# Performance work log

Measured on AMD Instinct MI355X. Metric: run time of the kernel, lower is better.

## Reference

```python
import jax, jax.numpy as jnp
import numpy as np

EPS = 1e-6      # l2_norm / denom clamp eps
BN_EPS = 1e-5   # BatchNorm eps


def _l2norm(x):
    # torch.norm(p=2, dim=-2, keepdim=True).clamp_min(eps)
    n = jnp.sqrt(jnp.sum(x * x, axis=-2, keepdims=True))
    return x / jnp.maximum(n, EPS)


def setup_inputs() -> dict:
    key = jax.random.key(0)
    ks = jax.random.split(key, 9)
    B, Cin_each, Co, H, W = 4, 256, 256, 128, 128
    Cq = Co // 8  # in_places // scale
    Cin = 4 * Cin_each
    return {
        "s5": jax.random.normal(ks[0], (B, Cin_each, H, W), jnp.float32),
        "s4": jax.random.normal(ks[1], (B, Cin_each, H, W), jnp.float32),
        "s3": jax.random.normal(ks[2], (B, Cin_each, H, W), jnp.float32),
        "s2": jax.random.normal(ks[3], (B, Cin_each, H, W), jnp.float32),
        # ConvBnRelu: 1x1 conv (no bias) + BN affine params
        "w_conv": jax.random.normal(ks[4], (Co, Cin), jnp.float32) * 0.03,
        "bn_gamma": jnp.ones((Co,), jnp.float32),
        "bn_beta": jnp.zeros((Co,), jnp.float32),
        # Attention 1x1 convs (with bias)
        "wq": jax.random.normal(ks[5], (Cq, Co), jnp.float32) * 0.06,
        "bq": jnp.zeros((Cq,), jnp.float32),
        "wk": jax.random.normal(ks[6], (Cq, Co), jnp.float32) * 0.06,
        "bk": jnp.zeros((Cq,), jnp.float32),
        "wv": jax.random.normal(ks[7], (Co, Co), jnp.float32) * 0.06,
        "bv": jnp.zeros((Co,), jnp.float32),
        # gamma is Parameter(zeros(1)) in the source; set nonzero so the
        # attention branch contributes to the output for kernel testing.
        "gamma": jnp.array(0.5, jnp.float32),
    }


def reference(s5, s4, s3, s2, w_conv, bn_gamma, bn_beta,
              wq, bq, wk, bk, wv, bv, gamma):
    # --- ConvBnRelu (1x1 conv, train-mode BN, ReLU) ---
    fcat = jnp.concatenate([s5, s4, s3, s2], axis=1)            # [B, 4C, H, W]
    x = jnp.einsum('oc,bchw->bohw', w_conv, fcat)               # 1x1 conv
    mu = x.mean(axis=(0, 2, 3), keepdims=True)
    var = x.var(axis=(0, 2, 3), keepdims=True)                  # biased, as torch BN
    x = (x - mu) / jnp.sqrt(var + BN_EPS)
    x = x * bn_gamma[None, :, None, None] + bn_beta[None, :, None, None]
    feat = jax.nn.relu(x)                                       # [B, C, H, W]

    # --- linear Attention (L2-norm QK, KV trick, no softmax) ---
    B, C, H, W = feat.shape
    N = H * W
    X = feat.reshape(B, C, N)
    Q = jnp.einsum('qc,bcn->bqn', wq, X) + bq[None, :, None]    # [B, Cq, N]
    K = jnp.einsum('qc,bcn->bqn', wk, X) + bk[None, :, None]    # [B, Cq, N]
    V = jnp.einsum('oc,bcn->bon', wv, X) + bv[None, :, None]    # [B, C, N]

    Qn = _l2norm(Q)                                             # norm over channel dim
    Kn = _l2norm(K)

    # denom: N + Q . sum_n K
    e = jnp.einsum('bqn,bq->bn', Qn, Kn.sum(axis=-1))           # [B, N]
    tailor = 1.0 / jnp.maximum(jnp.asarray(N, Qn.dtype) + e, 1e-6)

    # KV trick: [B, Cq, C] then project back through Q
    matrix = jnp.einsum('bqn,bcn->bqc', Kn, V)                  # [B, Cq, C]
    matrix_sum = V.sum(axis=-1)[:, :, None] + \
        jnp.einsum('bqn,bqc->bcn', Qn, matrix)                  # [B, C, N]

    weight_value = matrix_sum * tailor[:, None, :]              # [B, C, N]
    out = gamma * weight_value.reshape(B, C, H, W)
    out = jnp.nan_to_num(out, nan=0.0, posinf=1.0, neginf=-1.0)

    return out + feat
```

## Files before the change

kernel.cpp:

```cpp
#include <hip/hip_runtime.h>

#define B_   4
#define CO   256
#define CIN  1024
#define CQ   32
#define HN   16384
#define NPIX 65536
#define NTOT ((size_t)B_ * CO * HN)

typedef unsigned short ushort_t;
typedef __attribute__((ext_vector_type(8))) short bf16x8;
typedef __attribute__((ext_vector_type(4))) float f32x4;

__device__ __forceinline__ unsigned bf16pair(float x, float y) {
    unsigned xu = __float_as_uint(x), yu = __float_as_uint(y);
    unsigned xr = (xu + 0x7FFFu + ((xu >> 16) & 1u)) >> 16;
    unsigned yr = (yu + 0x7FFFu + ((yu >> 16) & 1u)) >> 16;
    return xr | (yr << 16);
}
__device__ __forceinline__ ushort_t bf16of(float x) {
    unsigned u = __float_as_uint(x);
    return (ushort_t)((u + 0x7FFFu + ((u >> 16) & 1u)) >> 16);
}
__device__ __forceinline__ float bf2f(ushort_t h) {
    return __uint_as_float(((unsigned)h) << 16);
}
__device__ __forceinline__ void unpack8(uint4 u, float* f) {
    f[0] = __uint_as_float(u.x << 16); f[1] = __uint_as_float(u.x & 0xffff0000u);
    f[2] = __uint_as_float(u.y << 16); f[3] = __uint_as_float(u.y & 0xffff0000u);
    f[4] = __uint_as_float(u.z << 16); f[5] = __uint_as_float(u.z & 0xffff0000u);
    f[6] = __uint_as_float(u.w << 16); f[7] = __uint_as_float(u.w & 0xffff0000u);
}
__device__ __forceinline__ void async16(void* lds, const void* g) {
    __builtin_amdgcn_global_load_lds(
        (const __attribute__((address_space(1))) void*)g,
        (__attribute__((address_space(3))) void*)lds, 16, 0, 0);
}

__global__ __launch_bounds__(256) void wcvt(
    const float* __restrict__ w, const float* __restrict__ wq,
    const float* __restrict__ wk, const float* __restrict__ wv,
    ushort_t* __restrict__ w_bf, ushort_t* __restrict__ wqk_bf,
    ushort_t* __restrict__ wv_bf)
{
    int i = blockIdx.x * 256 + threadIdx.x;
    if (i < 262144) {
        w_bf[i] = bf16of(w[i]);
    } else if (i < 278528) {
        int l = i - 262144; int row = l >> 8, col = l & 255;
        float v = (row < 32) ? wq[row * 256 + col] : wk[(row - 32) * 256 + col];
        wqk_bf[l] = bf16of(v);
    } else {
        int l = i - 278528;
        wv_bf[l] = bf16of(wv[l]);
    }
}

__global__ __launch_bounds__(256) void conv_mfma2(
    const float* __restrict__ s5, const float* __restrict__ s4,
    const float* __restrict__ s3, const float* __restrict__ s2,
    const ushort_t* __restrict__ w_bf, ushort_t* __restrict__ xb)
{
    __shared__ ushort_t Aw[128 * 32];
    __shared__ ushort_t Bf[32 * 130];
    const int o0 = blockIdx.x * 128;
    const int n0 = blockIdx.y * 128;
    const int b  = blockIdx.z;
    const int tid = threadIdx.x;
    const int wave = tid >> 6, lane = tid & 63, l15 = lane & 15, quad = lane >> 4;
    const int wm = wave & 1, wn = wave >> 1;
    f32x4 acc[4][4] = {};

    for (int k0 = 0; k0 < CIN; k0 += 32) {
        #pragma unroll
        for (int r = 0; r < 2; ++r) {
            int row = r * 64 + wave * 16;
            const ushort_t* g = w_bf + (size_t)(o0 + row + (lane >> 2)) * CIN
                                + k0 + (lane & 3) * 8;
            async16(&Aw[row * 32], g);
        }
        const int t = k0 >> 8;
        const float* src = ((t == 0) ? s5 : (t == 1) ? s4 : (t == 2) ? s3 : s2)
                           + ((size_t)b * 256 + (k0 & 255)) * HN + n0;
        #pragma unroll
        for (int i = 0; i < 4; ++i) {
            int gi = tid + 256 * i;
            int k = gi >> 5, n4 = gi & 31;
            float4 u = *(const float4*)(src + (size_t)k * HN + n4 * 4);
            *(unsigned*)&Bf[k * 130 + n4 * 4]     = bf16pair(u.x, u.y);
            *(unsigned*)&Bf[k * 130 + n4 * 4 + 2] = bf16pair(u.z, u.w);
        }
        __syncthreads();
        bf16x8 af[4], bfv[4];
        #pragma unroll
        for (int tm = 0; tm < 4; ++tm)
            af[tm] = *(const bf16x8*)&Aw[(wm * 64 + tm * 16 + l15) * 32 + quad * 8];
        #pragma unroll
        for (int tn = 0; tn < 4; ++tn) {
            int nl = wn * 64 + tn * 16 + l15;
            bf16x8 bb;
            #pragma unroll
            for (int j = 0; j < 8; ++j) bb[j] = (short)Bf[(quad * 8 + j) * 130 + nl];
            bfv[tn] = bb;
        }
        #pragma unroll
        for (int tm = 0; tm < 4; ++tm)
            #pragma unroll
            for (int tn = 0; tn < 4; ++tn)
                acc[tm][tn] = __builtin_amdgcn_mfma_f32_16x16x32_bf16(
                    af[tm], bfv[tn], acc[tm][tn], 0, 0, 0);
        __syncthreads();
    }
    #pragma unroll
    for (int tm = 0; tm < 4; ++tm)
        #pragma unroll
        for (int r = 0; r < 4; ++r) {
            int o = o0 + wm * 64 + tm * 16 + quad * 4 + r;
            size_t base = ((size_t)b * CO + o) * HN + n0;
            #pragma unroll
            for (int tn = 0; tn < 4; ++tn)
                xb[base + wn * 64 + tn * 16 + l15] = bf16of(acc[tm][tn][r]);
        }
}

__global__ __launch_bounds__(256) void bn_stats(
    const ushort_t* __restrict__ xb, float* __restrict__ accum)
{
    const int o = blockIdx.x, seg = blockIdx.y, tid = threadIdx.x;
    const int wave = tid >> 6, lane = tid & 63;
    float s = 0.f, ss = 0.f;
    for (int b = 0; b < B_; ++b) {
        const ushort_t* p = xb + ((size_t)(b * CO + o)) * HN + seg * 2048 + tid * 8;
        uint4 u = *(const uint4*)p;
        float f[8]; unpack8(u, f);
        #pragma unroll
        for (int j = 0; j < 8; ++j) { s += f[j]; ss += f[j] * f[j]; }
    }
    #pragma unroll
    for (int m = 1; m < 64; m <<= 1) { s += __shfl_xor(s, m); ss += __shfl_xor(ss, m); }
    __shared__ float shs[4], shss[4];
    if (lane == 0) { shs[wave] = s; shss[wave] = ss; }
    __syncthreads();
    if (tid == 0) {
        atomicAdd(&accum[o],       shs[0] + shs[1] + shs[2] + shs[3]);
        atomicAdd(&accum[256 + o], shss[0] + shss[1] + shss[2] + shss[3]);
    }
}

__global__ __launch_bounds__(256) void bn_finalize(
    const float* __restrict__ accum, const float* __restrict__ g,
    const float* __restrict__ bt, float* __restrict__ scale,
    float* __restrict__ shift)
{
    int o = threadIdx.x;
    float mu  = accum[o] / (float)NPIX;
    float var = accum[256 + o] / (float)NPIX - mu * mu;
    float sc  = g[o] * rsqrtf(var + 1e-5f);
    scale[o] = sc;
    shift[o] = bt[o] - mu * sc;
}

__global__ __launch_bounds__(256) void bnrelu_t(
    const ushort_t* __restrict__ xb, const float* __restrict__ scale,
    const float* __restrict__ shift, ushort_t* __restrict__ featT)
{
    __shared__ ushort_t sh[64 * 68];
    const int hn0 = blockIdx.x * 64, c0 = blockIdx.y * 64, b = blockIdx.z;
    const int tid = threadIdx.x;
    {
        int cl = tid >> 2, seg = tid & 3;
        float sc = scale[c0 + cl], sf = shift[c0 + cl];
        const ushort_t* src = xb + ((size_t)(b * CO + c0 + cl)) * HN + hn0 + seg * 16;
        #pragma unroll
        for (int h = 0; h < 2; ++h) {
            uint4 u = *(const uint4*)(src + h * 8);
            float f[8]; unpack8(u, f);
            #pragma unroll
            for (int j = 0; j < 8; ++j) {
                float v = fmaxf(fmaf(sc, f[j], sf), 0.f);
                sh[(seg * 16 + h * 8 + j) * 68 + cl] = bf16of(v);
            }
        }
    }
    __syncthreads();
    {
        int nl = tid >> 2, seg = tid & 3;
        size_t gn = (size_t)b * HN + hn0 + nl;
        ushort_t* dst = featT + gn * CO + c0 + seg * 16;
        #pragma unroll
        for (int j = 0; j < 4; ++j)
            *(uint2*)(dst + j * 4) = *(const uint2*)&sh[nl * 68 + seg * 16 + j * 4];
    }
}

__global__ __launch_bounds__(256) void qk_mfma(
    const ushort_t* __restrict__ featT, const ushort_t* __restrict__ wqk_bf,
    const float* __restrict__ bq, const float* __restrict__ bk,
    ushort_t* __restrict__ Qt, ushort_t* __restrict__ Kt,
    float* __restrict__ Ksum)
{
    __shared__ ushort_t At[128 * 32];
    __shared__ ushort_t Bt[64 * 32];
    const int n0 = blockIdx.x * 128;
    const int b  = n0 >> 14;
    const int tid = threadIdx.x;
    const int wave = tid >> 6, lane = tid & 63, l15 = lane & 15, quad = lane >> 4;
    const int nsub = (wave & 1) * 64;
    const int isK  = wave >> 1;
    f32x4 acc[4][2] = {};

    for (int k0 = 0; k0 < CO; k0 += 32) {
        #pragma unroll
        for (int r = 0; r < 2; ++r) {
            int row = r * 64 + wave * 16;
            const ushort_t* g = featT + (size_t)(n0 + row + (lane >> 2)) * CO
                                + k0 + (lane & 3) * 8;
            async16(&At[row * 32], g);
        }
        {
            int row = wave * 16;
            const ushort_t* g = wqk_bf + (size_t)(row + (lane >> 2)) * CO
                                + k0 + (lane & 3) * 8;
            async16(&Bt[row * 32], g);
        }
        __syncthreads();
        bf16x8 af[4], bfv[2];
        #pragma unroll
        for (int tm = 0; tm < 4; ++tm)
            af[tm] = *(const bf16x8*)&At[(nsub + tm * 16 + l15) * 32 + quad * 8];
        #pragma unroll
        for (int tc = 0; tc < 2; ++tc)
            bfv[tc] = *(const bf16x8*)&Bt[(isK * 32 + tc * 16 + l15) * 32 + quad * 8];
        #pragma unroll
        for (int tm = 0; tm < 4; ++tm)
            #pragma unroll
            for (int tc = 0; tc < 2; ++tc)
                acc[tm][tc] = __builtin_amdgcn_mfma_f32_16x16x32_bf16(
                    af[tm], bfv[tc], acc[tm][tc], 0, 0, 0);
        __syncthreads();
    }
    const float bias0 = isK ? bk[l15]      : bq[l15];
    const float bias1 = isK ? bk[16 + l15] : bq[16 + l15];
    ushort_t* dst = isK ? Kt : Qt;
    float ks0 = 0.f, ks1 = 0.f;
    #pragma unroll
    for (int tm = 0; tm < 4; ++tm)
        #pragma unroll
        for (int r = 0; r < 4; ++r) {
            float v0 = acc[tm][0][r] + bias0;
            float v1 = acc[tm][1][r] + bias1;
            float sq = v0 * v0 + v1 * v1;
            sq += __shfl_xor(sq, 1); sq += __shfl_xor(sq, 2);
            sq += __shfl_xor(sq, 4); sq += __shfl_xor(sq, 8);
            float inv = 1.f / fmaxf(sqrtf(sq), 1e-6f);
            v0 *= inv; v1 *= inv;
            int n = n0 + nsub + tm * 16 + quad * 4 + r;
            dst[(size_t)n * CQ + l15]      = bf16of(v0);
            dst[(size_t)n * CQ + 16 + l15] = bf16of(v1);
            ks0 += v0; ks1 += v1;
        }
    if (isK) {
        ks0 += __shfl_xor(ks0, 16); ks0 += __shfl_xor(ks0, 32);
        ks1 += __shfl_xor(ks1, 16); ks1 += __shfl_xor(ks1, 32);
        if (quad == 0) {
            atomicAdd(&Ksum[b * CQ + l15],      ks0);
            atomicAdd(&Ksum[b * CQ + 16 + l15], ks1);
        }
    }
}

__global__ __launch_bounds__(256) void v_mfma2(
    const ushort_t* __restrict__ featT, const ushort_t* __restrict__ wv_bf,
    const float* __restrict__ bv, ushort_t* __restrict__ Vt,
    float* __restrict__ Vsum)
{
    __shared__ ushort_t At[128 * 32];
    __shared__ ushort_t Bt[128 * 32];
    const int n0  = blockIdx.x * 128;
    const int co0 = blockIdx.y * 128;
    const int b   = n0 >> 14;
    const int tid = threadIdx.x;
    const int wave = tid >> 6, lane = tid & 63, l15 = lane & 15, quad = lane >> 4;
    const int wm = wave & 1, wn = wave >> 1;
    f32x4 acc[4][4] = {};

    for (int k0 = 0; k0 < CO; k0 += 32) {
        #pragma unroll
        for (int r = 0; r < 2; ++r) {
            int row = r * 64 + wave * 16;
            const ushort_t* ga = featT + (size_t)(n0 + row + (lane >> 2)) * CO
                                 + k0 + (lane & 3) * 8;
            async16(&At[row * 32], ga);
            const ushort_t* gb = wv_bf + (size_t)(co0 + row + (lane >> 2)) * CO
                                 + k0 + (lane & 3) * 8;
            async16(&Bt[row * 32], gb);
        }
        __syncthreads();
        bf16x8 af[4], bfv[4];
        #pragma unroll
        for (int tm = 0; tm < 4; ++tm)
            af[tm] = *(const bf16x8*)&At[(wm * 64 + tm * 16 + l15) * 32 + quad * 8];
        #pragma unroll
        for (int tn = 0; tn < 4; ++tn)
            bfv[tn] = *(const bf16x8*)&Bt[(wn * 64 + tn * 16 + l15) * 32 + quad * 8];
        #pragma unroll
        for (int tm = 0; tm < 4; ++tm)
            #pragma unroll
            for (int tn = 0; tn < 4; ++tn)
                acc[tm][tn] = __builtin_amdgcn_mfma_f32_16x16x32_bf16(
                    af[tm], bfv[tn], acc[tm][tn], 0, 0, 0);
        __syncthreads();
    }
    float bvl[4], vsum_p[4] = {};
    #pragma unroll
    for (int tn = 0; tn < 4; ++tn) bvl[tn] = bv[co0 + wn * 64 + tn * 16 + l15];
    #pragma unroll
    for (int tm = 0; tm < 4; ++tm)
        #pragma unroll
        for (int r = 0; r < 4; ++r) {
            int n = n0 + wm * 64 + tm * 16 + quad * 4 + r;
            size_t rb = (size_t)n * CO;
            #pragma unroll
            for (int tn = 0; tn < 4; ++tn) {
                float val = acc[tm][tn][r] + bvl[tn];
                Vt[rb + co0 + wn * 64 + tn * 16 + l15] = bf16of(val);
                vsum_p[tn] += val;
            }
        }
    #pragma unroll
    for (int tn = 0; tn < 4; ++tn) {
        float s = vsum_p[tn];
        s += __shfl_xor(s, 16); s += __shfl_xor(s, 32);
        if (quad == 0)
            atomicAdd(&Vsum[b * CO + co0 + wn * 64 + tn * 16 + l15], s);
    }
}

__global__ __launch_bounds__(256) void kv_outer(
    const ushort_t* __restrict__ Kt, const ushort_t* __restrict__ Vt,
    float* __restrict__ matT)
{
    __shared__ float k_s[32 * 36];
    __shared__ float v_s[32 * 268];
    const int chunk = blockIdx.x;
    const int b  = chunk >> 6;
    const int nb = chunk * 256;
    const int tid = threadIdx.x;
    const int tq = tid >> 5, tc = tid & 31;
    float acc[4][8] = {};

    for (int slab = 0; slab < 8; ++slab) {
        int ns = nb + slab * 32;
        {
            int nn = tid >> 3, qs = tid & 7;
            uint2 u = *(const uint2*)&Kt[(size_t)(ns + nn) * CQ + qs * 4];
            k_s[nn * 36 + qs * 4 + 0] = __uint_as_float(u.x << 16);
            k_s[nn * 36 + qs * 4 + 1] = __uint_as_float(u.x & 0xffff0000u);
            k_s[nn * 36 + qs * 4 + 2] = __uint_as_float(u.y << 16);
            k_s[nn * 36 + qs * 4 + 3] = __uint_as_float(u.y & 0xffff0000u);
        }
        #pragma unroll
        for (int p = 0; p < 4; ++p) {
            int nn = p * 8 + (tid & 7), cs = tid >> 3;
            uint4 u = *(const uint4*)&Vt[(size_t)(ns + nn) * CO + cs * 8];
            float f[8]; unpack8(u, f);
            *(float4*)&v_s[nn * 268 + cs * 8]     = make_float4(f[0], f[1], f[2], f[3]);
            *(float4*)&v_s[nn * 268 + cs * 8 + 4] = make_float4(f[4], f[5], f[6], f[7]);
        }
        __syncthreads();
        #pragma unroll 4
        for (int nn = 0; nn < 32; ++nn) {
            float4 kq = *(const float4*)&k_s[nn * 36 + tq * 4];
            float vv[8];
            #pragma unroll
            for (int ci = 0; ci < 8; ++ci) vv[ci] = v_s[nn * 268 + tc + 32 * ci];
            #pragma unroll
            for (int ci = 0; ci < 8; ++ci) {
                acc[0][ci] += kq.x * vv[ci];
                acc[1][ci] += kq.y * vv[ci];
                acc[2][ci] += kq.z * vv[ci];
                acc[3][ci] += kq.w * vv[ci];
            }
        }
        __syncthreads();
    }
    #pragma unroll
    for (int qi = 0; qi < 4; ++qi)
        #pragma unroll
        for (int ci = 0; ci < 8; ++ci)
            atomicAdd(&matT[b * 8192 + (tc + 32 * ci) * CQ + tq * 4 + qi],
                      acc[qi][ci]);
}

__global__ __launch_bounds__(256) void tailor_k(
    const ushort_t* __restrict__ Qt, const float* __restrict__ Ksum,
    float* __restrict__ tailor)
{
    __shared__ float ks[CQ];
    const int n = blockIdx.x * 256 + threadIdx.x;
    const int b = n >> 14;
    if (threadIdx.x < CQ) ks[threadIdx.x] = Ksum[b * CQ + threadIdx.x];
    __syncthreads();
    const uint4* q = (const uint4*)&Qt[(size_t)n * CQ];
    float e = 0.f;
    #pragma unroll
    for (int i = 0; i < 4; ++i) {
        float f[8]; unpack8(q[i], f);
        #pragma unroll
        for (int j = 0; j < 8; ++j) e += f[j] * ks[i * 8 + j];
    }
    tailor[n] = 1.f / fmaxf((float)HN + e, 1e-6f);
}

__global__ __launch_bounds__(256) void final_mfma(
    const ushort_t* __restrict__ xb, const ushort_t* __restrict__ Qt,
    const float* __restrict__ matT, const float* __restrict__ Vsum,
    const float* __restrict__ tailor, const float* __restrict__ scale,
    const float* __restrict__ shift, const float* __restrict__ gamma_p,
    float* __restrict__ out)
{
    const int c0 = blockIdx.x * 128;
    const int n0 = blockIdx.y * 128;
    const int b  = n0 >> 14, hn0 = n0 & 16383;
    const int tid = threadIdx.x;
    const int wave = tid >> 6, lane = tid & 63, l15 = lane & 15, quad = lane >> 4;
    const int wm = wave & 1, wn = wave >> 1;
    const float gamma = gamma_p[0];

    bf16x8 af[4], bfv[4];
    #pragma unroll
    for (int tm = 0; tm < 4; ++tm) {
        int c = c0 + wm * 64 + tm * 16 + l15;
        const float* mp = matT + b * 8192 + c * CQ + quad * 8;
        float4 m0 = *(const float4*)mp;
        float4 m1 = *(const float4*)(mp + 4);
        union { bf16x8 v; unsigned u[4]; } t;
        t.u[0] = bf16pair(m0.x, m0.y); t.u[1] = bf16pair(m0.z, m0.w);
        t.u[2] = bf16pair(m1.x, m1.y); t.u[3] = bf16pair(m1.z, m1.w);
        af[tm] = t.v;
    }
    #pragma unroll
    for (int tn = 0; tn < 4; ++tn) {
        int n = n0 + wn * 64 + tn * 16 + l15;
        bfv[tn] = *(const bf16x8*)&Qt[(size_t)n * CQ + quad * 8];
    }
    f32x4 acc[4][4] = {};
    #pragma unroll
    for (int tm = 0; tm < 4; ++tm)
        #pragma unroll
        for (int tn = 0; tn < 4; ++tn)
            acc[tm][tn] = __builtin_amdgcn_mfma_f32_16x16x32_bf16(
                af[tm], bfv[tn], acc[tm][tn], 0, 0, 0);

    float tl[4];
    #pragma unroll
    for (int tn = 0; tn < 4; ++tn) tl[tn] = tailor[n0 + wn * 64 + tn * 16 + l15];

    #pragma unroll
    for (int tm = 0; tm < 4; ++tm)
        #pragma unroll
        for (int r = 0; r < 4; ++r) {
            int c = c0 + wm * 64 + tm * 16 + quad * 4 + r;
            float vs = Vsum[b * CO + c];
            float sc = scale[c], sf = shift[c];
            size_t rowbase = ((size_t)(b * CO + c)) * HN + hn0;
            #pragma unroll
            for (int tn = 0; tn < 4; ++tn) {
                int nl = wn * 64 + tn * 16 + l15;
                float val = gamma * (acc[tm][tn][r] + vs) * tl[tn];
                if (isnan(val)) val = 0.f;
                else if (isinf(val)) val = (val > 0.f) ? 1.f : -1.f;
                float feat = fmaxf(fmaf(sc, bf2f(xb[rowbase + nl]), sf), 0.f);
                out[rowbase + nl] = val + feat;
            }
        }
}

extern "C" void kernel_launch(void* const* d_in, const int* in_sizes, int n_in,
                              void* d_out, int out_size, void* d_ws, size_t ws_size,
                              hipStream_t stream)
{
    const float* s5      = (const float*)d_in[0];
    const float* s4      = (const float*)d_in[1];
    const float* s3      = (const float*)d_in[2];
    const float* s2      = (const float*)d_in[3];
    const float* w_conv  = (const float*)d_in[4];
    const float* bn_g    = (const float*)d_in[5];
    const float* bn_b    = (const float*)d_in[6];
    const float* wq      = (const float*)d_in[7];
    const float* bq      = (const float*)d_in[8];
    const float* wk      = (const float*)d_in[9];
    const float* bk      = (const float*)d_in[10];
    const float* wv      = (const float*)d_in[11];
    const float* bv      = (const float*)d_in[12];
    const float* gamma_p = (const float*)d_in[13];

    char* p = (char*)d_ws;
    ushort_t* xb     = (ushort_t*)p;  p += NTOT * 2;
    ushort_t* featT  = (ushort_t*)p;  p += NTOT * 2;
    ushort_t* Qt     = (ushort_t*)p;  p += (size_t)NPIX * CQ * 2;
    ushort_t* Kt     = (ushort_t*)p;  p += (size_t)NPIX * CQ * 2;
    ushort_t* w_bf   = (ushort_t*)p;  p += (size_t)CO * CIN * 2;
    ushort_t* wqk_bf = (ushort_t*)p;  p += 64 * CO * 2;
    ushort_t* wv_bf  = (ushort_t*)p;  p += (size_t)CO * CO * 2;
    float* matT  = (float*)p;
    float* Ksum  = matT + (size_t)B_ * CO * CQ;
    float* Vsum  = Ksum + B_ * CQ;
    float* accum = Vsum + B_ * CO;
    size_t zero_bytes = (size_t)(32768 + 128 + 1024 + 512) * 4;
    p += zero_bytes;
    float* scale  = (float*)p;  p += 256 * 4;
    float* shift  = (float*)p;  p += 256 * 4;
    float* tailor = (float*)p;  p += (size_t)NPIX * 4;

    hipMemsetAsync(matT, 0, zero_bytes, stream);
    wcvt<<<1344, 256, 0, stream>>>(w_conv, wq, wk, wv, w_bf, wqk_bf, wv_bf);
    conv_mfma2<<<dim3(2, 128, B_), 256, 0, stream>>>(s5, s4, s3, s2, w_bf, xb);
    bn_stats<<<dim3(256, 8), 256, 0, stream>>>(xb, accum);
    bn_finalize<<<1, 256, 0, stream>>>(accum, bn_g, bn_b, scale, shift);
    bnrelu_t<<<dim3(256, 4, B_), 256, 0, stream>>>(xb, scale, shift, featT);
    qk_mfma<<<512, 256, 0, stream>>>(featT, wqk_bf, bq, bk, Qt, Kt, Ksum);
    v_mfma2<<<dim3(512, 2), 256, 0, stream>>>(featT, wv_bf, bv, (ushort_t*)d_out, Vsum);
    kv_outer<<<256, 256, 0, stream>>>(Kt, (const ushort_t*)d_out, matT);
    tailor_k<<<256, 256, 0, stream>>>(Qt, Ksum, tailor);
    final_mfma<<<dim3(2, 512), 256, 0, stream>>>(xb, Qt, matT, Vsum, tailor,
                                                 scale, shift, gamma_p,
                                                 (float*)d_out);
}
```

Baseline: 516.9 us.

## Double-buffer conv GEMM with swizzled LDS and fuse KV product into V GEMM

The 1x1 conv GEMM now double-buffers its weight and activation tiles. It prefetches the next K slice into registers while the MFMAs run, and it uses XOR-swizzled, k-contiguous LDS layouts so B fragments are read as vector loads instead of scalar gathers. K is written channel-major (KtT) so it can feed MFMA directly. The V projection now keeps its tile in LDS and computes the K^T·V partial product with MFMAs, accumulating atomically into matT. This removes the V round-trip through global memory and the separate scalar-FMA kv_outer kernel. The cost is more LDS per block, strided K stores, and matT partials now computed from bf16 V via MFMA.

```diff
diff --git a/kernel.cpp b/kernel.cpp
--- a/kernel.cpp
+++ b/kernel.cpp
@@ -56,52 +56,78 @@
     }
 }
 
-__global__ __launch_bounds__(256) void conv_mfma2(
+__global__ __launch_bounds__(256) void conv_mfma3(
     const float* __restrict__ s5, const float* __restrict__ s4,
     const float* __restrict__ s3, const float* __restrict__ s2,
     const ushort_t* __restrict__ w_bf, ushort_t* __restrict__ xb)
 {
-    __shared__ ushort_t Aw[128 * 32];
-    __shared__ ushort_t Bf[32 * 130];
+    __shared__ ushort_t Aw[2][128 * 32];
+    __shared__ ushort_t Bn[2][128 * 40];
     const int o0 = blockIdx.x * 128;
     const int n0 = blockIdx.y * 128;
     const int b  = blockIdx.z;
     const int tid = threadIdx.x;
     const int wave = tid >> 6, lane = tid & 63, l15 = lane & 15, quad = lane >> 4;
     const int wm = wave & 1, wn = wave >> 1;
+    const int n_st = tid & 127;
+    const int kqb  = tid >> 7;
+    const int bswz = ((n_st >> 3) & 3) << 1;
     f32x4 acc[4][4] = {};
-
+    float v[4][4];
+
+    auto loadB = [&](int k0) {
+        const float* base = (k0 < 256) ? s5 : (k0 < 512) ? s4
+                          : (k0 < 768) ? s3 : s2;
+        const float* sp = base + ((size_t)b * 256 + (k0 & 255)) * HN + n0 + n_st;
+        #pragma unroll
+        for (int i = 0; i < 4; ++i) {
+            const float* cp = sp + (size_t)(kqb + 2 * i) * 4 * HN;
+            #pragma unroll
+            for (int j = 0; j < 4; ++j) v[i][j] = cp[(size_t)j * HN];
+        }
+    };
+    auto storeB = [&](int bi) {
+        ushort_t* Bp = Bn[bi];
+        #pragma unroll
+        for (int i = 0; i < 4; ++i) {
+            int pos = (kqb + 2 * i) ^ bswz;
+            uint2 u = make_uint2(bf16pair(v[i][0], v[i][1]),
+                                 bf16pair(v[i][2], v[i][3]));
+            *(uint2*)&Bp[n_st * 40 + pos * 4] = u;
+        }
+    };
+    auto issueA = [&](int k0, int bi) {
+        #pragma unroll
+        for (int r = 0; r < 2; ++r) {
+            int row  = r * 64 + wave * 16;
+            int orow = row + (lane >> 2);
+            const ushort_t* g = w_bf + (size_t)(o0 + orow) * CIN + k0
+                                + (((lane & 3) ^ ((orow >> 1) & 3)) << 3);
+            async16(&Aw[bi][row * 32], g);
+        }
+    };
+
+    issueA(0, 0);
+    loadB(0);
+    storeB(0);
+
+    int buf = 0;
     for (int k0 = 0; k0 < CIN; k0 += 32) {
-        #pragma unroll
-        for (int r = 0; r < 2; ++r) {
-            int row = r * 64 + wave * 16;
-            const ushort_t* g = w_bf + (size_t)(o0 + row + (lane >> 2)) * CIN
-                                + k0 + (lane & 3) * 8;
-            async16(&Aw[row * 32], g);
-        }
-        const int t = k0 >> 8;
-        const float* src = ((t == 0) ? s5 : (t == 1) ? s4 : (t == 2) ? s3 : s2)
-                           + ((size_t)b * 256 + (k0 & 255)) * HN + n0;
-        #pragma unroll
-        for (int i = 0; i < 4; ++i) {
-            int gi = tid + 256 * i;
-            int k = gi >> 5, n4 = gi & 31;
-            float4 u = *(const float4*)(src + (size_t)k * HN + n4 * 4);
-            *(unsigned*)&Bf[k * 130 + n4 * 4]     = bf16pair(u.x, u.y);
-            *(unsigned*)&Bf[k * 130 + n4 * 4 + 2] = bf16pair(u.z, u.w);
-        }
         __syncthreads();
+        const bool more = (k0 + 32 < CIN);
+        if (more) { issueA(k0 + 32, buf ^ 1); loadB(k0 + 32); }
         bf16x8 af[4], bfv[4];
         #pragma unroll
-        for (int tm = 0; tm < 4; ++tm)
-            af[tm] = *(const bf16x8*)&Aw[(wm * 64 + tm * 16 + l15) * 32 + quad * 8];
+        for (int tm = 0; tm < 4; ++tm) {
+            int orow = wm * 64 + tm * 16 + l15;
+            int pos  = quad ^ ((orow >> 1) & 3);
+            af[tm] = *(const bf16x8*)&Aw[buf][orow * 32 + pos * 8];
+        }
         #pragma unroll
         for (int tn = 0; tn < 4; ++tn) {
             int nl = wn * 64 + tn * 16 + l15;
-            bf16x8 bb;
-            #pragma unroll
-            for (int j = 0; j < 8; ++j) bb[j] = (short)Bf[(quad * 8 + j) * 130 + nl];
-            bfv[tn] = bb;
+            int p0 = (2 * quad) ^ (((nl >> 3) & 3) << 1);
+            bfv[tn] = *(const bf16x8*)&Bn[buf][nl * 40 + p0 * 4];
         }
         #pragma unroll
         for (int tm = 0; tm < 4; ++tm)
@@ -109,7 +135,8 @@
             for (int tn = 0; tn < 4; ++tn)
                 acc[tm][tn] = __builtin_amdgcn_mfma_f32_16x16x32_bf16(
                     af[tm], bfv[tn], acc[tm][tn], 0, 0, 0);
-        __syncthreads();
+        if (more) storeB(buf ^ 1);
+        buf ^= 1;
     }
     #pragma unroll
     for (int tm = 0; tm < 4; ++tm)
@@ -196,13 +223,14 @@
 __global__ __launch_bounds__(256) void qk_mfma(
     const ushort_t* __restrict__ featT, const ushort_t* __restrict__ wqk_bf,
     const float* __restrict__ bq, const float* __restrict__ bk,
-    ushort_t* __restrict__ Qt, ushort_t* __restrict__ Kt,
+    ushort_t* __restrict__ Qt, ushort_t* __restrict__ KtT,
     float* __restrict__ Ksum)
 {
     __shared__ ushort_t At[128 * 32];
     __shared__ ushort_t Bt[64 * 32];
     const int n0 = blockIdx.x * 128;
     const int b  = n0 >> 14;
+    const int hn0 = n0 & 16383;
     const int tid = threadIdx.x;
     const int wave = tid >> 6, lane = tid & 63, l15 = lane & 15, quad = lane >> 4;
     const int nsub = (wave & 1) * 64;
@@ -241,7 +269,6 @@
     }
     const float bias0 = isK ? bk[l15]      : bq[l15];
     const float bias1 = isK ? bk[16 + l15] : bq[16 + l15];
-    ushort_t* dst = isK ? Kt : Qt;
     float ks0 = 0.f, ks1 = 0.f;
     #pragma unroll
     for (int tm = 0; tm < 4; ++tm)
@@ -254,9 +281,15 @@
             sq += __shfl_xor(sq, 4); sq += __shfl_xor(sq, 8);
             float inv = 1.f / fmaxf(sqrtf(sq), 1e-6f);
             v0 *= inv; v1 *= inv;
-            int n = n0 + nsub + tm * 16 + quad * 4 + r;
-            dst[(size_t)n * CQ + l15]      = bf16of(v0);
-            dst[(size_t)n * CQ + 16 + l15] = bf16of(v1);
+            if (isK) {
+                int hn = hn0 + nsub + tm * 16 + quad * 4 + r;
+                KtT[((size_t)(b * CQ + l15)) * HN + hn]      = bf16of(v0);
+                KtT[((size_t)(b * CQ + 16 + l15)) * HN + hn] = bf16of(v1);
+            } else {
+                int n = n0 + nsub + tm * 16 + quad * 4 + r;
+                Qt[(size_t)n * CQ + l15]      = bf16of(v0);
+                Qt[(size_t)n * CQ + 16 + l15] = bf16of(v1);
+            }
             ks0 += v0; ks1 += v1;
         }
     if (isK) {
@@ -269,16 +302,18 @@
     }
 }
 
-__global__ __launch_bounds__(256) void v_mfma2(
+__global__ __launch_bounds__(256) void v_kv_mfma(
     const ushort_t* __restrict__ featT, const ushort_t* __restrict__ wv_bf,
-    const float* __restrict__ bv, ushort_t* __restrict__ Vt,
-    float* __restrict__ Vsum)
-{
-    __shared__ ushort_t At[128 * 32];
-    __shared__ ushort_t Bt[128 * 32];
+    const float* __restrict__ bv, const ushort_t* __restrict__ KtT,
+    float* __restrict__ matT, float* __restrict__ Vsum)
+{
+    __shared__ ushort_t sh[128 * 136];
+    ushort_t* At = sh;
+    ushort_t* Bt = sh + 4096;
     const int n0  = blockIdx.x * 128;
     const int co0 = blockIdx.y * 128;
     const int b   = n0 >> 14;
+    const int hn0 = n0 & 16383;
     const int tid = threadIdx.x;
     const int wave = tid >> 6, lane = tid & 63, l15 = lane & 15, quad = lane >> 4;
     const int wm = wave & 1, wn = wave >> 1;
@@ -311,21 +346,23 @@
                     af[tm], bfv[tn], acc[tm][tn], 0, 0, 0);
         __syncthreads();
     }
+    ushort_t* Vlds = sh;
     float bvl[4], vsum_p[4] = {};
     #pragma unroll
     for (int tn = 0; tn < 4; ++tn) bvl[tn] = bv[co0 + wn * 64 + tn * 16 + l15];
     #pragma unroll
     for (int tm = 0; tm < 4; ++tm)
         #pragma unroll
-        for (int r = 0; r < 4; ++r) {
-            int n = n0 + wm * 64 + tm * 16 + quad * 4 + r;
-            size_t rb = (size_t)n * CO;
-            #pragma unroll
-            for (int tn = 0; tn < 4; ++tn) {
-                float val = acc[tm][tn][r] + bvl[tn];
-                Vt[rb + co0 + wn * 64 + tn * 16 + l15] = bf16of(val);
-                vsum_p[tn] += val;
-            }
+        for (int tn = 0; tn < 4; ++tn) {
+            float x0 = acc[tm][tn][0] + bvl[tn];
+            float x1 = acc[tm][tn][1] + bvl[tn];
+            float x2 = acc[tm][tn][2] + bvl[tn];
+            float x3 = acc[tm][tn][3] + bvl[tn];
+            vsum_p[tn] += (x0 + x1) + (x2 + x3);
+            uint2 u = make_uint2(bf16pair(x0, x1), bf16pair(x2, x3));
+            int c_loc = wn * 64 + tn * 16 + l15;
+            int nb    = wm * 64 + tm * 16 + quad * 4;
+            *(uint2*)&Vlds[c_loc * 136 + nb] = u;
         }
     #pragma unroll
     for (int tn = 0; tn < 4; ++tn) {
@@ -334,62 +371,36 @@
         if (quad == 0)
             atomicAdd(&Vsum[b * CO + co0 + wn * 64 + tn * 16 + l15], s);
     }
-}
-
-__global__ __launch_bounds__(256) void kv_outer(
-    const ushort_t* __restrict__ Kt, const ushort_t* __restrict__ Vt,
-    float* __restrict__ matT)
-{
-    __shared__ float k_s[32 * 36];
-    __shared__ float v_s[32 * 268];
-    const int chunk = blockIdx.x;
-    const int b  = chunk >> 6;
-    const int nb = chunk * 256;
-    const int tid = threadIdx.x;
-    const int tq = tid >> 5, tc = tid & 31;
-    float acc[4][8] = {};
-
-    for (int slab = 0; slab < 8; ++slab) {
-        int ns = nb + slab * 32;
-        {
-            int nn = tid >> 3, qs = tid & 7;
-            uint2 u = *(const uint2*)&Kt[(size_t)(ns + nn) * CQ + qs * 4];
-            k_s[nn * 36 + qs * 4 + 0] = __uint_as_float(u.x << 16);
-            k_s[nn * 36 + qs * 4 + 1] = __uint_as_float(u.x & 0xffff0000u);
-            k_s[nn * 36 + qs * 4 + 2] = __uint_as_float(u.y << 16);
-            k_s[nn * 36 + qs * 4 + 3] = __uint_as_float(u.y & 0xffff0000u);
-        }
-        #pragma unroll
-        for (int p = 0; p < 4; ++p) {
-            int nn = p * 8 + (tid & 7), cs = tid >> 3;
-            uint4 u = *(const uint4*)&Vt[(size_t)(ns + nn) * CO + cs * 8];
-            float f[8]; unpack8(u, f);
-            *(float4*)&v_s[nn * 268 + cs * 8]     = make_float4(f[0], f[1], f[2], f[3]);
-            *(float4*)&v_s[nn * 268 + cs * 8 + 4] = make_float4(f[4], f[5], f[6], f[7]);
-        }
-        __syncthreads();
-        #pragma unroll 4
-        for (int nn = 0; nn < 32; ++nn) {
-            float4 kq = *(const float4*)&k_s[nn * 36 + tq * 4];
-            float vv[8];
-            #pragma unroll
-            for (int ci = 0; ci < 8; ++ci) vv[ci] = v_s[nn * 268 + tc + 32 * ci];
-            #pragma unroll
-            for (int ci = 0; ci < 8; ++ci) {
-                acc[0][ci] += kq.x * vv[ci];
-                acc[1][ci] += kq.y * vv[ci];
-                acc[2][ci] += kq.z * vv[ci];
-                acc[3][ci] += kq.w * vv[ci];
+    __syncthreads();
+    f32x4 acc2[2][2] = {};
+    #pragma unroll
+    for (int ks = 0; ks < 4; ++ks) {
+        bf16x8 a2[2], b2[2];
+        #pragma unroll
+        for (int t2 = 0; t2 < 2; ++t2)
+            a2[t2] = *(const bf16x8*)&Vlds[(wave * 32 + t2 * 16 + l15) * 136
+                                           + ks * 32 + quad * 8];
+        #pragma unroll
+        for (int tc = 0; tc < 2; ++tc)
+            b2[tc] = *(const bf16x8*)&KtT[((size_t)(b * CQ + tc * 16 + l15)) * HN
+                                          + hn0 + ks * 32 + quad * 8];
+        #pragma unroll
+        for (int t2 = 0; t2 < 2; ++t2)
+            #pragma unroll
+            for (int tc = 0; tc < 2; ++tc)
+                acc2[t2][tc] = __builtin_amdgcn_mfma_f32_16x16x32_bf16(
+                    a2[t2], b2[tc], acc2[t2][tc], 0, 0, 0);
+    }
+    #pragma unroll
+    for (int t2 = 0; t2 < 2; ++t2)
+        #pragma unroll
+        for (int tc = 0; tc < 2; ++tc)
+            #pragma unroll
+            for (int r = 0; r < 4; ++r) {
+                int c = co0 + wave * 32 + t2 * 16 + quad * 4 + r;
+                atomicAdd(&matT[b * 8192 + c * CQ + tc * 16 + l15],
+                          acc2[t2][tc][r]);
             }
-        }
-        __syncthreads();
-    }
-    #pragma unroll
-    for (int qi = 0; qi < 4; ++qi)
-        #pragma unroll
-        for (int ci = 0; ci < 8; ++ci)
-            atomicAdd(&matT[b * 8192 + (tc + 32 * ci) * CQ + tq * 4 + qi],
-                      acc[qi][ci]);
 }
 
 __global__ __launch_bounds__(256) void tailor_k(
@@ -499,7 +510,7 @@
     ushort_t* xb     = (ushort_t*)p;  p += NTOT * 2;
     ushort_t* featT  = (ushort_t*)p;  p += NTOT * 2;
     ushort_t* Qt     = (ushort_t*)p;  p += (size_t)NPIX * CQ * 2;
-    ushort_t* Kt     = (ushort_t*)p;  p += (size_t)NPIX * CQ * 2;
+    ushort_t* KtT    = (ushort_t*)p;  p += (size_t)NPIX * CQ * 2;
     ushort_t* w_bf   = (ushort_t*)p;  p += (size_t)CO * CIN * 2;
     ushort_t* wqk_bf = (ushort_t*)p;  p += 64 * CO * 2;
     ushort_t* wv_bf  = (ushort_t*)p;  p += (size_t)CO * CO * 2;
@@ -515,14 +526,13 @@
 
     hipMemsetAsync(matT, 0, zero_bytes, stream);
     wcvt<<<1344, 256, 0, stream>>>(w_conv, wq, wk, wv, w_bf, wqk_bf, wv_bf);
-    conv_mfma2<<<dim3(2, 128, B_), 256, 0, stream>>>(s5, s4, s3, s2, w_bf, xb);
+    conv_mfma3<<<dim3(2, 128, B_), 256, 0, stream>>>(s5, s4, s3, s2, w_bf, xb);
     bn_stats<<<dim3(256, 8), 256, 0, stream>>>(xb, accum);
     bn_finalize<<<1, 256, 0, stream>>>(accum, bn_g, bn_b, scale, shift);
     bnrelu_t<<<dim3(256, 4, B_), 256, 0, stream>>>(xb, scale, shift, featT);
-    qk_mfma<<<512, 256, 0, stream>>>(featT, wqk_bf, bq, bk, Qt, Kt, Ksum);
-    v_mfma2<<<dim3(512, 2), 256, 0, stream>>>(featT, wv_bf, bv, (ushort_t*)d_out, Vsum);
-    kv_outer<<<256, 256, 0, stream>>>(Kt, (const ushort_t*)d_out, matT);
+    qk_mfma<<<512, 256, 0, stream>>>(featT, wqk_bf, bq, bk, Qt, KtT, Ksum);
     tailor_k<<<256, 256, 0, stream>>>(Qt, Ksum, tailor);
+    v_kv_mfma<<<dim3(512, 2), 256, 0, stream>>>(featT, wv_bf, bv, KtT, matT, Vsum);
     final_mfma<<<dim3(2, 512), 256, 0, stream>>>(xb, Qt, matT, Vsum, tailor,
                                                  scale, shift, gamma_p,
                                                  (float*)d_out);
```

New measurement: 422.5 us. 18.3% less time.
